# Performance work log

Hardware: AMD Instinct MI355X
Metric: run time of the kernel (lower is better)

## Reference

```python
import jax, jax.numpy as jnp
import numpy as np
import math

_LINK_MASK_VALUE = -1000000000.0
B, N, HID, NH = 8, 1024, 1024, 4
HD = HID // NH


def setup_inputs() -> dict:
    key = jax.random.key(0)
    ks = jax.random.split(key, 8)
    features = jax.random.normal(ks[0], (B, N, HID), dtype=jnp.float32)
    valid_mask = jax.random.bernoulli(ks[1], 0.9, (B, N))
    s = 0.02
    Wq = jax.random.normal(ks[2], (HID, HID), dtype=jnp.float32) * s
    bq = jnp.zeros((HID,), dtype=jnp.float32)
    Wk = jax.random.normal(ks[3], (HID, HID), dtype=jnp.float32) * s
    bk = jnp.zeros((HID,), dtype=jnp.float32)
    Wg = jax.random.normal(ks[4], (HID, NH), dtype=jnp.float32) * s
    bg = jnp.zeros((NH,), dtype=jnp.float32)
    return {"features": features, "valid_mask": valid_mask,
            "Wq": Wq, "bq": bq, "Wk": Wk, "bk": bk, "Wg": Wg, "bg": bg}


def reference(features, valid_mask, Wq, bq, Wk, bk, Wg, bg):
    b, n, _ = features.shape
    Q = (features @ Wq + bq).reshape(b, n, NH, HD)
    K = (features @ Wk + bk).reshape(b, n, NH, HD)
    log_gates = jax.nn.log_softmax(features @ Wg + bg, axis=-1)  # (b, n, H)
    scores = jnp.einsum('bihd,bjhd->bijh', Q, K) / math.sqrt(HD)  # (b, i, j, H)
    triu = jnp.triu(jnp.ones((n, n), dtype=bool), k=1)            # (n, n)
    tvm = triu[None, :, :] & valid_mask[:, None, :]               # (b, i, j)
    row_dead = ~jnp.any(tvm, axis=2, keepdims=True)               # (b, i, 1)
    tvm = tvm | row_dead
    scores = jnp.where(tvm[..., None], scores, _LINK_MASK_VALUE)
    log_per_head = jax.nn.log_softmax(scores, axis=2)             # softmax over j
    log_per_head = jnp.where(row_dead[..., None], _LINK_MASK_VALUE, log_per_head)
    # mixture over heads with per-row gates
    log_links = jax.scipy.special.logsumexp(log_per_head + log_gates[:, :, None, :], axis=-1)
    return log_links
```

## Files before the change

kernel.cpp:

```cpp
#include <hip/hip_runtime.h>


typedef __attribute__((ext_vector_type(8))) short bf16x8;
typedef __attribute__((ext_vector_type(4))) short bf16x4;
typedef __attribute__((ext_vector_type(4))) float f32x4;

#define LB __launch_bounds__(256)

__device__ __forceinline__ short f2bf(float f) {
    unsigned u = __float_as_uint(f);
    u += 0x7fffu + ((u >> 16) & 1u);
    return (short)(u >> 16);
}

__device__ __forceinline__ void gld16(const void* g, void* l) {
    __builtin_amdgcn_global_load_lds(
        (const __attribute__((address_space(1))) unsigned int*)g,
        (__attribute__((address_space(3))) unsigned int*)l, 16, 0, 0);
}

__global__ LB void k_prep2(const float* __restrict__ feat, const float* __restrict__ Wg,
                           const float* __restrict__ bg, const float* __restrict__ Wq,
                           const float* __restrict__ Wk, short* __restrict__ Xb,
                           float* __restrict__ lgA, short* __restrict__ Wt) {
    __shared__ float tile[32][33];
    const int t = threadIdx.x;
    if (blockIdx.x < 2048) {
        int row = blockIdx.x * 4 + (t >> 6);
        int lane = t & 63;
        const float* f = feat + (size_t)row * 1024;
        float g0 = 0.f, g1 = 0.f, g2 = 0.f, g3 = 0.f;
#pragma unroll
        for (int tt = 0; tt < 4; ++tt) {
            int k = tt * 256 + lane * 4;
            float4 x = *(const float4*)&f[k];
            float4 w0 = *(const float4*)&Wg[(k + 0) * 4];
            float4 w1 = *(const float4*)&Wg[(k + 1) * 4];
            float4 w2 = *(const float4*)&Wg[(k + 2) * 4];
            float4 w3 = *(const float4*)&Wg[(k + 3) * 4];
            g0 += x.x * w0.x + x.y * w1.x + x.z * w2.x + x.w * w3.x;
            g1 += x.x * w0.y + x.y * w1.y + x.z * w2.y + x.w * w3.y;
            g2 += x.x * w0.z + x.y * w1.z + x.z * w2.z + x.w * w3.z;
            g3 += x.x * w0.w + x.y * w1.w + x.z * w2.w + x.w * w3.w;
            bf16x4 xv;
            xv[0] = f2bf(x.x); xv[1] = f2bf(x.y); xv[2] = f2bf(x.z); xv[3] = f2bf(x.w);
            *(bf16x4*)&Xb[(size_t)row * 1024 + k] = xv;
        }
#pragma unroll
        for (int off = 32; off; off >>= 1) {
            g0 += __shfl_xor(g0, off); g1 += __shfl_xor(g1, off);
            g2 += __shfl_xor(g2, off); g3 += __shfl_xor(g3, off);
        }
        g0 += bg[0]; g1 += bg[1]; g2 += bg[2]; g3 += bg[3];
        float m = fmaxf(fmaxf(g0, g1), fmaxf(g2, g3));
        float s = __expf(g0 - m) + __expf(g1 - m) + __expf(g2 - m) + __expf(g3 - m);
        float ls = m + __logf(s);
        if (lane == 0) {
            float4 o = {g0 - ls, g1 - ls, g2 - ls, g3 - ls};
            *(float4*)&lgA[row * 4] = o;
        }
    } else {
        int bid = blockIdx.x - 2048;
        int n0 = (bid & 63) * 32, k0 = (bid >> 6) * 32;
        const float* W = (n0 < 1024) ? Wq : Wk;
        int nb = n0 & 1023;
        int tx = t & 31, ty = t >> 5;
#pragma unroll
        for (int jj = 0; jj < 4; ++jj) {
            int k = ty + jj * 8;
            tile[k][tx] = W[(size_t)(k0 + k) * 1024 + nb + tx];
        }
        __syncthreads();
#pragma unroll
        for (int jj = 0; jj < 4; ++jj) {
            int n = ty + jj * 8;
            Wt[(size_t)(n0 + n) * 1024 + k0 + tx] = f2bf(tile[tx][n]);
        }
    }
}

__global__ __launch_bounds__(512, 2) void k_gemm(const short* __restrict__ Xb,
                                                 const short* __restrict__ Wt,
                                                 const float* __restrict__ bq,
                                                 const float* __restrict__ bk,
                                                 short* __restrict__ Qb,
                                                 short* __restrict__ Kb) {
    __shared__ short As[2][16384];
    __shared__ short Bs[2][16384];
    const int t = threadIdx.x;
    const int lane = t & 63, wid = t >> 6;
    const int wr = wid >> 2, wc = wid & 3;
    const int lr = lane & 15, lg4 = lane >> 4;
    const int wgid = (blockIdx.x & 7) * 32 + (blockIdx.x >> 3);
    const int mt = wgid >> 3, nt = wgid & 7;
    const int m0t = mt * 256, n0t = nt * 256;

    f32x4 acc[8][4] = {};

#define STAGE_A(q, k1, dst)                                                     \
    { int s_ = (q) * 512 + t; int tr_ = s_ >> 3, sl_ = s_ & 7;                  \
      gld16(&Xb[(size_t)(m0t + tr_) * 1024 + (k1) + ((sl_ ^ (tr_ & 7)) * 8)],   \
            &(dst)[s_ * 8]); }
#define STAGE_B(q, k1, dst)                                                     \
    { int s_ = (q) * 512 + t; int tr_ = s_ >> 3, sl_ = s_ & 7;                  \
      gld16(&Wt[(size_t)(n0t + tr_) * 1024 + (k1) + ((sl_ ^ (tr_ & 7)) * 8)],   \
            &(dst)[s_ * 8]); }

    {
        short* Ad = As[0]; short* Bd = Bs[0];
        STAGE_A(0, 0, Ad); STAGE_A(1, 0, Ad); STAGE_A(2, 0, Ad); STAGE_A(3, 0, Ad);
        STAGE_B(0, 0, Bd); STAGE_B(1, 0, Bd); STAGE_B(2, 0, Bd); STAGE_B(3, 0, Bd);
    }
    asm volatile("s_waitcnt vmcnt(0)" ::: "memory");
    __builtin_amdgcn_sched_barrier(0);
    __builtin_amdgcn_s_barrier();

    for (int kt = 0; kt < 16; ++kt) {
        const int cur = kt & 1;
        const short* Ac = As[cur];
        const short* Bc = Bs[cur];
        short* Ad = As[cur ^ 1];
        short* Bd = Bs[cur ^ 1];
        const int k1 = (kt + 1) * 64;
#pragma unroll
        for (int p = 0; p < 4; ++p) {
            const int mh = p >> 1, nh = p & 1;
            bf16x8 aF[4][2], bF[2][2];
#pragma unroll
            for (int m = 0; m < 4; ++m)
#pragma unroll
                for (int ks = 0; ks < 2; ++ks) {
                    int row = wr * 128 + mh * 64 + m * 16 + lr;
                    aF[m][ks] = *(const bf16x8*)
                        &Ac[row * 64 + (((ks * 4 + lg4) ^ (lr & 7)) * 8)];
                }
#pragma unroll
            for (int n = 0; n < 2; ++n)
#pragma unroll
                for (int ks = 0; ks < 2; ++ks) {
                    int row = wc * 64 + (nh * 2 + n) * 16 + lr;
                    bF[n][ks] = *(const bf16x8*)
                        &Bc[row * 64 + (((ks * 4 + lg4) ^ (lr & 7)) * 8)];
                }
            if (kt < 15) {
                if (p == 0)      { STAGE_A(0, k1, Ad); STAGE_A(2, k1, Ad); }
                else if (p == 1) { STAGE_B(0, k1, Bd); STAGE_B(1, k1, Bd); }
                else if (p == 2) { STAGE_B(2, k1, Bd); STAGE_B(3, k1, Bd); }
                else             { STAGE_A(1, k1, Ad); STAGE_A(3, k1, Ad); }
            }
            if (p == 1) {
                if (kt < 15) asm volatile("s_waitcnt vmcnt(4)" ::: "memory");
                else         asm volatile("s_waitcnt vmcnt(0)" ::: "memory");
            } else if (p == 3 && kt < 15) {
                asm volatile("s_waitcnt vmcnt(2)" ::: "memory");
            }
            __builtin_amdgcn_sched_barrier(0);
            __builtin_amdgcn_s_barrier();
            asm volatile("s_waitcnt lgkmcnt(0)" ::: "memory");
            __builtin_amdgcn_sched_barrier(0);
            __builtin_amdgcn_s_setprio(1);
#pragma unroll
            for (int ks = 0; ks < 2; ++ks)
#pragma unroll
                for (int m = 0; m < 4; ++m)
#pragma unroll
                    for (int n = 0; n < 2; ++n)
                        acc[mh * 4 + m][nh * 2 + n] =
                            __builtin_amdgcn_mfma_f32_16x16x32_bf16(
                                aF[m][ks], bF[n][ks], acc[mh * 4 + m][nh * 2 + n],
                                0, 0, 0);
            __builtin_amdgcn_s_setprio(0);
        }
    }
#undef STAGE_A
#undef STAGE_B

#pragma unroll
    for (int mf = 0; mf < 8; ++mf) {
#pragma unroll
        for (int nf = 0; nf < 4; ++nf) {
            int col = n0t + wc * 64 + nf * 16 + lr;
            float bias = (col < 1024) ? bq[col] : bk[col - 1024];
            float scale = (col < 1024) ? 0.0625f : 1.0f;
            short* dst = (col < 1024) ? Qb : Kb;
            int h = (col >> 8) & 3, d = col & 255;
#pragma unroll
            for (int r = 0; r < 4; ++r) {
                int rowg = m0t + wr * 128 + mf * 16 + lg4 * 4 + r;
                int b_ = rowg >> 10, i_ = rowg & 1023;
                float v = (acc[mf][nf][r] + bias) * scale;
                dst[((size_t)(b_ * 4 + h) * 1024 + i_) * 256 + d] = f2bf(v);
            }
        }
    }
}

__global__ __launch_bounds__(256, 2) void k_sc(const short* __restrict__ Qb,
                                               const short* __restrict__ Kb,
                                               const int* __restrict__ vm,
                                               char* __restrict__ Pe8,
                                               float* __restrict__ Zp) {
    __shared__ short SMEM[32768];
    short* As0 = SMEM;
    short* Bs0 = SMEM + 16384;
    const int t = threadIdx.x;
    const int lane = t & 63, wid = t >> 6;
    const int wr = wid >> 1, wc = wid & 1;
    const int lr = lane & 15, lg4 = lane >> 4;
    const int gidx = (blockIdx.x & 7) * 144 + (blockIdx.x >> 3);
    const int bh = gidx / 36, tt = gidx % 36;
    const int it8 = (tt >= 8) + (tt >= 15) + (tt >= 21) + (tt >= 26)
                  + (tt >= 30) + (tt >= 33) + (tt >= 35);
    const int base8 = (it8 == 0) ? 0 : (it8 == 1) ? 8 : (it8 == 2) ? 15
                    : (it8 == 3) ? 21 : (it8 == 4) ? 26 : (it8 == 5) ? 30
                    : (it8 == 6) ? 33 : 35;
    const int jt8 = it8 + (tt - base8);
    const int b = bh >> 2;
    const short* Qp = Qb + ((size_t)bh << 18);
    const short* Kp = Kb + ((size_t)bh << 18);

    f32x4 acc[4][4] = {};

#define SCA(q, k1, dst)                                                         \
    { int s_ = (q) * 256 + t; int tr_ = s_ >> 3, sl_ = s_ & 7;                  \
      gld16(&Qp[(size_t)(it8 * 128 + tr_) * 256 + (k1) + ((sl_ ^ (tr_ & 7)) * 8)], \
            &(dst)[s_ * 8]); }
#define SCB(q, k1, dst)                                                         \
    { int s_ = (q) * 256 + t; int tr_ = s_ >> 3, sl_ = s_ & 7;                  \
      gld16(&Kp[(size_t)(jt8 * 128 + tr_) * 256 + (k1) + ((sl_ ^ (tr_ & 7)) * 8)], \
            &(dst)[s_ * 8]); }

    {
        short* Ad = As0; short* Bd = Bs0;
        SCA(0, 0, Ad); SCA(1, 0, Ad); SCA(2, 0, Ad); SCA(3, 0, Ad);
        SCB(0, 0, Bd); SCB(1, 0, Bd); SCB(2, 0, Bd); SCB(3, 0, Bd);
    }
    asm volatile("s_waitcnt vmcnt(0)" ::: "memory");
    __builtin_amdgcn_sched_barrier(0);
    __builtin_amdgcn_s_barrier();

    for (int kt = 0; kt < 4; ++kt) {
        const int cur = kt & 1;
        const short* Ac = As0 + cur * 8192;
        const short* Bc = Bs0 + cur * 8192;
        short* Ad = As0 + (cur ^ 1) * 8192;
        short* Bd = Bs0 + (cur ^ 1) * 8192;
        const int k1 = (kt + 1) * 64;
        bf16x8 aF[2][2], bF[4][2];
#pragma unroll
        for (int m = 0; m < 2; ++m)
#pragma unroll
            for (int ks = 0; ks < 2; ++ks) {
                int row = wr * 64 + m * 16 + lr;
                aF[m][ks] = *(const bf16x8*)
                    &Ac[row * 64 + (((ks * 4 + lg4) ^ (lr & 7)) * 8)];
            }
#pragma unroll
        for (int n = 0; n < 4; ++n)
#pragma unroll
            for (int ks = 0; ks < 2; ++ks) {
                int row = wc * 64 + n * 16 + lr;
                bF[n][ks] = *(const bf16x8*)
                    &Bc[row * 64 + (((ks * 4 + lg4) ^ (lr & 7)) * 8)];
            }
        if (kt < 3) { SCA(0, k1, Ad); SCA(2, k1, Ad); SCB(0, k1, Bd); SCB(2, k1, Bd); }
        if (kt < 3) asm volatile("s_waitcnt vmcnt(4)" ::: "memory");
        else        asm volatile("s_waitcnt vmcnt(0)" ::: "memory");
        __builtin_amdgcn_sched_barrier(0);
        __builtin_amdgcn_s_barrier();
        asm volatile("s_waitcnt lgkmcnt(0)" ::: "memory");
        __builtin_amdgcn_sched_barrier(0);
        __builtin_amdgcn_s_setprio(1);
#pragma unroll
        for (int ks = 0; ks < 2; ++ks)
#pragma unroll
            for (int m = 0; m < 2; ++m)
#pragma unroll
                for (int n = 0; n < 4; ++n)
                    acc[m][n] = __builtin_amdgcn_mfma_f32_16x16x32_bf16(
                        aF[m][ks], bF[n][ks], acc[m][n], 0, 0, 0);
        __builtin_amdgcn_s_setprio(0);
#pragma unroll
        for (int m = 0; m < 2; ++m)
#pragma unroll
            for (int ks = 0; ks < 2; ++ks) {
                int row = wr * 64 + 32 + m * 16 + lr;
                aF[m][ks] = *(const bf16x8*)
                    &Ac[row * 64 + (((ks * 4 + lg4) ^ (lr & 7)) * 8)];
            }
        if (kt < 3) {
            SCB(1, k1, Bd); SCB(3, k1, Bd); SCA(1, k1, Ad); SCA(3, k1, Ad);
            asm volatile("s_waitcnt vmcnt(2)" ::: "memory");
            __builtin_amdgcn_sched_barrier(0);
        }
        __builtin_amdgcn_s_barrier();
        asm volatile("s_waitcnt lgkmcnt(0)" ::: "memory");
        __builtin_amdgcn_sched_barrier(0);
        __builtin_amdgcn_s_setprio(1);
#pragma unroll
        for (int ks = 0; ks < 2; ++ks)
#pragma unroll
            for (int m = 0; m < 2; ++m)
#pragma unroll
                for (int n = 0; n < 4; ++n)
                    acc[2 + m][n] = __builtin_amdgcn_mfma_f32_16x16x32_bf16(
                        aF[m][ks], bF[n][ks], acc[2 + m][n], 0, 0, 0);
        __builtin_amdgcn_s_setprio(0);
    }
#undef SCA
#undef SCB

    __syncthreads();
    char* wbuf = (char*)SMEM + wid * 5120;
    char* Pp = Pe8 + ((size_t)bh << 20);
    const int rowbase = it8 * 128 + wr * 64;
    const int colbase = jt8 * 128 + wc * 64;
    int vmv[4];
#pragma unroll
    for (int nf = 0; nf < 4; ++nf)
        vmv[nf] = vm[(b << 10) + colbase + nf * 16 + lr];
    float zacc[4][4] = {};
#pragma unroll
    for (int m4 = 0; m4 < 4; ++m4) {
#pragma unroll
        for (int nf = 0; nf < 4; ++nf) {
            const int col = colbase + nf * 16 + lr;
            float e0 = __expf(acc[m4][nf][0]);
            float e1 = __expf(acc[m4][nf][1]);
            float e2 = __expf(acc[m4][nf][2]);
            float e3 = __expf(acc[m4][nf][3]);
            const int row0 = rowbase + m4 * 16 + lg4 * 4;
            zacc[m4][0] += (vmv[nf] && (col > row0 + 0)) ? e0 : 0.f;
            zacc[m4][1] += (vmv[nf] && (col > row0 + 1)) ? e1 : 0.f;
            zacc[m4][2] += (vmv[nf] && (col > row0 + 2)) ? e2 : 0.f;
            zacc[m4][3] += (vmv[nf] && (col > row0 + 3)) ? e3 : 0.f;
            unsigned u01 = (unsigned)__builtin_amdgcn_cvt_pk_fp8_f32(e0, e1, 0, false);
            unsigned u23 = (unsigned)__builtin_amdgcn_cvt_pk_fp8_f32(e2, e3, 0, false);
            const int lrow = m4 * 16 + lg4 * 4;
            const int lcol = nf * 16 + lr;
            wbuf[(lrow + 0) * 80 + lcol] = (char)(u01 & 0xff);
            wbuf[(lrow + 1) * 80 + lcol] = (char)((u01 >> 8) & 0xff);
            wbuf[(lrow + 2) * 80 + lcol] = (char)(u23 & 0xff);
            wbuf[(lrow + 3) * 80 + lcol] = (char)((u23 >> 8) & 0xff);
        }
    }
#pragma unroll
    for (int c = 0; c < 4; ++c) {
        const int rrow = c * 16 + (lane >> 2);
        uint4 v = *(const uint4*)&wbuf[rrow * 80 + (lane & 3) * 16];
        const int grow = rowbase + rrow;
        if (colbase + 63 > grow)
            *(uint4*)&Pp[(size_t)grow * 1024 + colbase + (lane & 3) * 16] = v;
    }
#pragma unroll
    for (int m4 = 0; m4 < 4; ++m4)
#pragma unroll
        for (int r = 0; r < 4; ++r) {
            zacc[m4][r] += __shfl_xor(zacc[m4][r], 1);
            zacc[m4][r] += __shfl_xor(zacc[m4][r], 2);
            zacc[m4][r] += __shfl_xor(zacc[m4][r], 4);
            zacc[m4][r] += __shfl_xor(zacc[m4][r], 8);
        }
    if (lr == 0) {
        float* Zs = Zp + (size_t)(jt8 * 2 + wc) * 32768 + bh * 1024;
#pragma unroll
        for (int m4 = 0; m4 < 4; ++m4)
#pragma unroll
            for (int r = 0; r < 4; ++r)
                Zs[rowbase + m4 * 16 + lg4 * 4 + r] = zacc[m4][r];
    }
}

__global__ LB void k_final(const char* __restrict__ Pe8, const int* __restrict__ vm,
                           const float* __restrict__ lgA, const float* __restrict__ Zp,
                           float* __restrict__ out) {
    __shared__ float ecs[4];
    const int blk = blockIdx.x;
    const int b = blk >> 10, i = blk & 1023;
    const int t = threadIdx.x;
    if (t < 64) {
        int h = t >> 4, sl = t & 15;
        int base = (b * 4 + h) * 1024 + i;
        float z = (sl >= ((i >> 7) << 1)) ? Zp[(size_t)sl * 32768 + base] : 0.f;
        z += __shfl_xor(z, 1); z += __shfl_xor(z, 2);
        z += __shfl_xor(z, 4); z += __shfl_xor(z, 8);
        if (sl == 0) {
            float lgv = lgA[blk * 4 + h];
            ecs[h] = (z > 0.f) ? __expf(lgv) / z : 0.f;
        }
    }
    __syncthreads();
    const int j0 = t * 4;
    float4 o = {-1.0e9f, -1.0e9f, -1.0e9f, -1.0e9f};
    if (j0 + 3 > i) {
        int4 v4 = *(const int4*)&vm[(b << 10) + j0];
        float a0 = 0.f, a1 = 0.f, a2 = 0.f, a3 = 0.f;
#pragma unroll
        for (int h = 0; h < 4; ++h) {
            unsigned p = *(const unsigned*)
                &Pe8[(((size_t)(b * 4 + h)) << 20) + ((size_t)i << 10) + j0];
            float ech = ecs[h];
            a0 += __builtin_amdgcn_cvt_f32_fp8((int)p, 0) * ech;
            a1 += __builtin_amdgcn_cvt_f32_fp8((int)p, 1) * ech;
            a2 += __builtin_amdgcn_cvt_f32_fp8((int)p, 2) * ech;
            a3 += __builtin_amdgcn_cvt_f32_fp8((int)p, 3) * ech;
        }
        o.x = (v4.x && (j0 + 0 > i)) ? __logf(a0) : -1.0e9f;
        o.y = (v4.y && (j0 + 1 > i)) ? __logf(a1) : -1.0e9f;
        o.z = (v4.z && (j0 + 2 > i)) ? __logf(a2) : -1.0e9f;
        o.w = (v4.w && (j0 + 3 > i)) ? __logf(a3) : -1.0e9f;
    }
    *(float4*)&out[((size_t)blk << 10) + j0] = o;
}

extern "C" void kernel_launch(void* const* d_in, const int* in_sizes, int n_in,
                              void* d_out, int out_size, void* d_ws, size_t ws_size,
                              hipStream_t stream) {
    const float* features = (const float*)d_in[0];
    const int*   vmask    = (const int*)d_in[1];
    const float* Wq       = (const float*)d_in[2];
    const float* bq       = (const float*)d_in[3];
    const float* Wk       = (const float*)d_in[4];
    const float* bk       = (const float*)d_in[5];
    const float* Wg       = (const float*)d_in[6];
    const float* bg       = (const float*)d_in[7];
    float* out = (float*)d_out;

    char*  Pe8 = (char*)d_ws;
    short* Xb = (short*)d_ws;
    short* Wt = Xb + 8388608;
    short* Qb = (short*)d_ws + 33554432;
    short* Kb = Qb + 8388608;
    float* lgA = (float*)(Kb + 8388608);
    float* Zp  = lgA + 32768;

    k_prep2<<<4096, 256, 0, stream>>>(features, Wg, bg, Wq, Wk, Xb, lgA, Wt);
    k_gemm<<<256, 512, 0, stream>>>(Xb, Wt, bq, bk, Qb, Kb);
    k_sc<<<1152, 256, 0, stream>>>(Qb, Kb, vmask, Pe8, Zp);
    k_final<<<8192, 256, 0, stream>>>(Pe8, vmask, lgA, Zp, out);
}
```

Before: 92.59 us.

## Switch QK projection GEMM to FP8 MFMA with triple-buffered LDS pipeline

Features and transposed weights are now quantized to FP8 (weights pre-scaled by 16) instead of bf16, and the projection GEMM uses the 32x32x64 scaled f8f6f4 MFMA with a three-stage LDS ring and a new swizzle. This halves GEMM operand bytes and doubles MFMA throughput per instruction. It also cuts prep-kernel write traffic. The risk is FP8 precision loss in Q/K, which feed a log-softmax over scores and could exceed tolerance.

```diff
diff --git a/kernel.cpp b/kernel.cpp
--- a/kernel.cpp
+++ b/kernel.cpp
@@ -4,6 +4,8 @@
 typedef __attribute__((ext_vector_type(8))) short bf16x8;
 typedef __attribute__((ext_vector_type(4))) short bf16x4;
 typedef __attribute__((ext_vector_type(4))) float f32x4;
+typedef __attribute__((ext_vector_type(16))) float f32x16;
+typedef __attribute__((ext_vector_type(8))) int i32x8;
 
 #define LB __launch_bounds__(256)
 
@@ -21,8 +23,8 @@
 
 __global__ LB void k_prep2(const float* __restrict__ feat, const float* __restrict__ Wg,
                            const float* __restrict__ bg, const float* __restrict__ Wq,
-                           const float* __restrict__ Wk, short* __restrict__ Xb,
-                           float* __restrict__ lgA, short* __restrict__ Wt) {
+                           const float* __restrict__ Wk, char* __restrict__ X8,
+                           float* __restrict__ lgA, char* __restrict__ W8) {
     __shared__ float tile[32][33];
     const int t = threadIdx.x;
     if (blockIdx.x < 2048) {
@@ -42,9 +44,9 @@
             g1 += x.x * w0.y + x.y * w1.y + x.z * w2.y + x.w * w3.y;
             g2 += x.x * w0.z + x.y * w1.z + x.z * w2.z + x.w * w3.z;
             g3 += x.x * w0.w + x.y * w1.w + x.z * w2.w + x.w * w3.w;
-            bf16x4 xv;
-            xv[0] = f2bf(x.x); xv[1] = f2bf(x.y); xv[2] = f2bf(x.z); xv[3] = f2bf(x.w);
-            *(bf16x4*)&Xb[(size_t)row * 1024 + k] = xv;
+            unsigned u01 = (unsigned)__builtin_amdgcn_cvt_pk_fp8_f32(x.x, x.y, 0, false);
+            unsigned u23 = (unsigned)__builtin_amdgcn_cvt_pk_fp8_f32(x.z, x.w, 0, false);
+            *(unsigned*)&X8[(size_t)row * 1024 + k] = (u01 & 0xffffu) | (u23 << 16);
         }
 #pragma unroll
         for (int off = 32; off; off >>= 1) {
@@ -74,121 +76,99 @@
 #pragma unroll
         for (int jj = 0; jj < 4; ++jj) {
             int n = ty + jj * 8;
-            Wt[(size_t)(n0 + n) * 1024 + k0 + tx] = f2bf(tile[tx][n]);
-        }
-    }
-}
-
-__global__ __launch_bounds__(512, 2) void k_gemm(const short* __restrict__ Xb,
-                                                 const short* __restrict__ Wt,
+            float w16 = tile[tx][n] * 16.f;
+            W8[(size_t)(n0 + n) * 1024 + k0 + tx] =
+                (char)(__builtin_amdgcn_cvt_pk_fp8_f32(w16, w16, 0, false) & 0xff);
+        }
+    }
+}
+
+__device__ __forceinline__ i32x8 ldfrag8(const char* tb, int row, int khalf) {
+    const int sw = (row >> 1) & 3;
+    uint4 lo = *(const uint4*)&tb[row * 64 + (((khalf * 2 + 0) ^ sw) * 16)];
+    uint4 hi = *(const uint4*)&tb[row * 64 + (((khalf * 2 + 1) ^ sw) * 16)];
+    i32x8 r;
+    r[0] = lo.x; r[1] = lo.y; r[2] = lo.z; r[3] = lo.w;
+    r[4] = hi.x; r[5] = hi.y; r[6] = hi.z; r[7] = hi.w;
+    return r;
+}
+
+__global__ __launch_bounds__(512, 2) void k_gemm(const char* __restrict__ X8,
+                                                 const char* __restrict__ W8,
                                                  const float* __restrict__ bq,
                                                  const float* __restrict__ bk,
                                                  short* __restrict__ Qb,
                                                  short* __restrict__ Kb) {
-    __shared__ short As[2][16384];
-    __shared__ short Bs[2][16384];
+    __shared__ char SM[3][32768];
     const int t = threadIdx.x;
     const int lane = t & 63, wid = t >> 6;
     const int wr = wid >> 2, wc = wid & 3;
-    const int lr = lane & 15, lg4 = lane >> 4;
+    const int l31 = lane & 31, khalf = lane >> 5;
     const int wgid = (blockIdx.x & 7) * 32 + (blockIdx.x >> 3);
-    const int mt = wgid >> 3, nt = wgid & 7;
-    const int m0t = mt * 256, n0t = nt * 256;
-
-    f32x4 acc[8][4] = {};
-
-#define STAGE_A(q, k1, dst)                                                     \
-    { int s_ = (q) * 512 + t; int tr_ = s_ >> 3, sl_ = s_ & 7;                  \
-      gld16(&Xb[(size_t)(m0t + tr_) * 1024 + (k1) + ((sl_ ^ (tr_ & 7)) * 8)],   \
-            &(dst)[s_ * 8]); }
-#define STAGE_B(q, k1, dst)                                                     \
-    { int s_ = (q) * 512 + t; int tr_ = s_ >> 3, sl_ = s_ & 7;                  \
-      gld16(&Wt[(size_t)(n0t + tr_) * 1024 + (k1) + ((sl_ ^ (tr_ & 7)) * 8)],   \
-            &(dst)[s_ * 8]); }
-
-    {
-        short* Ad = As[0]; short* Bd = Bs[0];
-        STAGE_A(0, 0, Ad); STAGE_A(1, 0, Ad); STAGE_A(2, 0, Ad); STAGE_A(3, 0, Ad);
-        STAGE_B(0, 0, Bd); STAGE_B(1, 0, Bd); STAGE_B(2, 0, Bd); STAGE_B(3, 0, Bd);
-    }
-    asm volatile("s_waitcnt vmcnt(0)" ::: "memory");
+    const int m0t = (wgid >> 3) * 256, n0t = (wgid & 7) * 256;
+
+    f32x16 acc[4][2] = {};
+
+#define SGA(q, k1, dst)                                                         \
+    { int s_ = (q) * 512 + t; int tr_ = s_ >> 2, c_ = s_ & 3;                   \
+      gld16(&X8[(size_t)(m0t + tr_) * 1024 + (k1) + (((c_) ^ ((tr_ >> 1) & 3)) * 16)], \
+            (dst) + s_ * 16); }
+#define SGB(q, k1, dst)                                                         \
+    { int s_ = (q) * 512 + t; int tr_ = s_ >> 2, c_ = s_ & 3;                   \
+      gld16(&W8[(size_t)(n0t + tr_) * 1024 + (k1) + (((c_) ^ ((tr_ >> 1) & 3)) * 16)], \
+            (dst) + 16384 + s_ * 16); }
+
+    SGA(0, 0, SM[0]); SGA(1, 0, SM[0]); SGB(0, 0, SM[0]); SGB(1, 0, SM[0]);
+    SGA(0, 64, SM[1]); SGA(1, 64, SM[1]); SGB(0, 64, SM[1]); SGB(1, 64, SM[1]);
+    asm volatile("s_waitcnt vmcnt(4)" ::: "memory");
     __builtin_amdgcn_sched_barrier(0);
     __builtin_amdgcn_s_barrier();
 
     for (int kt = 0; kt < 16; ++kt) {
-        const int cur = kt & 1;
-        const short* Ac = As[cur];
-        const short* Bc = Bs[cur];
-        short* Ad = As[cur ^ 1];
-        short* Bd = Bs[cur ^ 1];
-        const int k1 = (kt + 1) * 64;
-#pragma unroll
-        for (int p = 0; p < 4; ++p) {
-            const int mh = p >> 1, nh = p & 1;
-            bf16x8 aF[4][2], bF[2][2];
-#pragma unroll
-            for (int m = 0; m < 4; ++m)
-#pragma unroll
-                for (int ks = 0; ks < 2; ++ks) {
-                    int row = wr * 128 + mh * 64 + m * 16 + lr;
-                    aF[m][ks] = *(const bf16x8*)
-                        &Ac[row * 64 + (((ks * 4 + lg4) ^ (lr & 7)) * 8)];
-                }
-#pragma unroll
-            for (int n = 0; n < 2; ++n)
-#pragma unroll
-                for (int ks = 0; ks < 2; ++ks) {
-                    int row = wc * 64 + (nh * 2 + n) * 16 + lr;
-                    bF[n][ks] = *(const bf16x8*)
-                        &Bc[row * 64 + (((ks * 4 + lg4) ^ (lr & 7)) * 8)];
-                }
-            if (kt < 15) {
-                if (p == 0)      { STAGE_A(0, k1, Ad); STAGE_A(2, k1, Ad); }
-                else if (p == 1) { STAGE_B(0, k1, Bd); STAGE_B(1, k1, Bd); }
-                else if (p == 2) { STAGE_B(2, k1, Bd); STAGE_B(3, k1, Bd); }
-                else             { STAGE_A(1, k1, Ad); STAGE_A(3, k1, Ad); }
-            }
-            if (p == 1) {
-                if (kt < 15) asm volatile("s_waitcnt vmcnt(4)" ::: "memory");
-                else         asm volatile("s_waitcnt vmcnt(0)" ::: "memory");
-            } else if (p == 3 && kt < 15) {
-                asm volatile("s_waitcnt vmcnt(2)" ::: "memory");
-            }
-            __builtin_amdgcn_sched_barrier(0);
-            __builtin_amdgcn_s_barrier();
-            asm volatile("s_waitcnt lgkmcnt(0)" ::: "memory");
-            __builtin_amdgcn_sched_barrier(0);
-            __builtin_amdgcn_s_setprio(1);
-#pragma unroll
-            for (int ks = 0; ks < 2; ++ks)
-#pragma unroll
-                for (int m = 0; m < 4; ++m)
-#pragma unroll
-                    for (int n = 0; n < 2; ++n)
-                        acc[mh * 4 + m][nh * 2 + n] =
-                            __builtin_amdgcn_mfma_f32_16x16x32_bf16(
-                                aF[m][ks], bF[n][ks], acc[mh * 4 + m][nh * 2 + n],
-                                0, 0, 0);
-            __builtin_amdgcn_s_setprio(0);
-        }
-    }
-#undef STAGE_A
-#undef STAGE_B
-
-#pragma unroll
-    for (int mf = 0; mf < 8; ++mf) {
-#pragma unroll
-        for (int nf = 0; nf < 4; ++nf) {
-            int col = n0t + wc * 64 + nf * 16 + lr;
-            float bias = (col < 1024) ? bq[col] : bk[col - 1024];
-            float scale = (col < 1024) ? 0.0625f : 1.0f;
+        const char* buf = SM[kt % 3];
+        char* bufn = SM[(kt + 2) % 3];
+        if (kt < 14) {
+            const int k2 = (kt + 2) * 64;
+            SGA(0, k2, bufn); SGA(1, k2, bufn); SGB(0, k2, bufn); SGB(1, k2, bufn);
+        }
+        i32x8 aF[4], bF[2];
+#pragma unroll
+        for (int rt = 0; rt < 4; ++rt)
+            aF[rt] = ldfrag8(buf, wr * 128 + rt * 32 + l31, khalf);
+#pragma unroll
+        for (int ct = 0; ct < 2; ++ct)
+            bF[ct] = ldfrag8(buf + 16384, wc * 64 + ct * 32 + l31, khalf);
+        __builtin_amdgcn_s_setprio(1);
+#pragma unroll
+        for (int rt = 0; rt < 4; ++rt)
+#pragma unroll
+            for (int ct = 0; ct < 2; ++ct)
+                acc[rt][ct] = __builtin_amdgcn_mfma_scale_f32_32x32x64_f8f6f4(
+                    aF[rt], bF[ct], acc[rt][ct], 0, 0, 0, 127, 0, 127);
+        __builtin_amdgcn_s_setprio(0);
+        if (kt < 14)       asm volatile("s_waitcnt vmcnt(4)" ::: "memory");
+        else if (kt == 14) asm volatile("s_waitcnt vmcnt(0)" ::: "memory");
+        __builtin_amdgcn_sched_barrier(0);
+        __builtin_amdgcn_s_barrier();
+    }
+#undef SGA
+#undef SGB
+
+#pragma unroll
+    for (int rt = 0; rt < 4; ++rt) {
+#pragma unroll
+        for (int ct = 0; ct < 2; ++ct) {
+            const int col = n0t + wc * 64 + ct * 32 + l31;
+            const float bias = (col < 1024) ? bq[col] : bk[col - 1024];
+            const float scale = (col < 1024) ? 0.0625f : 1.0f;
             short* dst = (col < 1024) ? Qb : Kb;
-            int h = (col >> 8) & 3, d = col & 255;
-#pragma unroll
-            for (int r = 0; r < 4; ++r) {
-                int rowg = m0t + wr * 128 + mf * 16 + lg4 * 4 + r;
-                int b_ = rowg >> 10, i_ = rowg & 1023;
-                float v = (acc[mf][nf][r] + bias) * scale;
+            const int h = (col >> 8) & 3, d = col & 255;
+#pragma unroll
+            for (int reg = 0; reg < 16; ++reg) {
+                const int rin = (reg & 3) + 8 * (reg >> 2) + 4 * khalf;
+                const int grow = m0t + wr * 128 + rt * 32 + rin;
+                const int b_ = grow >> 10, i_ = grow & 1023;
+                float v = (acc[rt][ct][reg] * 0.0625f + bias) * scale;
                 dst[((size_t)(b_ * 4 + h) * 1024 + i_) * 256 + d] = f2bf(v);
             }
         }
@@ -427,15 +407,15 @@
     float* out = (float*)d_out;
 
     char*  Pe8 = (char*)d_ws;
-    short* Xb = (short*)d_ws;
-    short* Wt = Xb + 8388608;
-    short* Qb = (short*)d_ws + 33554432;
+    char*  X8  = (char*)d_ws;
+    char*  W8  = X8 + 8388608;
+    short* Qb = (short*)((char*)d_ws + 33554432);
     short* Kb = Qb + 8388608;
     float* lgA = (float*)(Kb + 8388608);
     float* Zp  = lgA + 32768;
 
-    k_prep2<<<4096, 256, 0, stream>>>(features, Wg, bg, Wq, Wk, Xb, lgA, Wt);
-    k_gemm<<<256, 512, 0, stream>>>(Xb, Wt, bq, bk, Qb, Kb);
+    k_prep2<<<4096, 256, 0, stream>>>(features, Wg, bg, Wq, Wk, X8, lgA, W8);
+    k_gemm<<<256, 512, 0, stream>>>(X8, W8, bq, bk, Qb, Kb);
     k_sc<<<1152, 256, 0, stream>>>(Qb, Kb, vmask, Pe8, Zp);
     k_final<<<8192, 256, 0, stream>>>(Pe8, vmask, lgA, Zp, out);
 }
```

After: 80.81 us. -12.7%, faster.
